# Kernel optimization log

Measured on AMD Instinct MI355X. Metric: run time of the kernel, lower is better.

The kernel has to match this reference:

```python
import jax, jax.numpy as jnp
import numpy as np


def _cos_map(N):
    # DCT-II basis: weight[n, x] = cos(n*(x+0.5)/N*pi)*sqrt(2/N), row 0 scaled by 1/sqrt(2)
    pos = (jnp.arange(N, dtype=jnp.float32) + 0.5) / N
    n = jnp.arange(N, dtype=jnp.float32)[:, None]
    w = jnp.cos(n * pos[None, :] * jnp.pi) * np.sqrt(2.0 / N)
    return w.at[0].multiply(1.0 / np.sqrt(2.0))


def _dct3(x, cT, cH, cW):
    # x: [B,C,T,H,W]; matmul(x, cos.T) along each axis
    x = jnp.einsum('bcthw,Ww->bcthW', x, cW)
    x = jnp.einsum('bcthw,Hh->bctHw', x, cH)
    x = jnp.einsum('bcthw,Tt->bcThw', x, cT)
    return x


def _idct3(x, cT, cH, cW):
    # matmul(x, cos) along each axis
    x = jnp.einsum('bcthw,wW->bcthW', x, cW)
    x = jnp.einsum('bcthw,hH->bctHw', x, cH)
    x = jnp.einsum('bcthw,tT->bcThw', x, cT)
    return x


def setup_inputs() -> dict:
    key = jax.random.key(0)
    ks = jax.random.split(key, 12)
    B, C, T, H, W = 2, 96, 16, 64, 64
    hd = 96
    s = 0.02
    return {
        'x': jax.random.normal(ks[0], (B, C, T, H, W), jnp.float32),
        'freq_embed': jax.random.normal(ks[1], (T, H, W, hd), jnp.float32),
        'dwconv_w': jax.random.normal(ks[2], (hd, 1, 3, 3, 3), jnp.float32) * s,
        'dwconv_b': jnp.zeros((hd,), jnp.float32),
        'linear_w': jax.random.normal(ks[3], (2 * hd, hd), jnp.float32) * s,
        'linear_b': jnp.zeros((2 * hd,), jnp.float32),
        'v0_w': jax.random.normal(ks[4], (hd, hd), jnp.float32) * s,
        'v0_b': jnp.zeros((hd,), jnp.float32),
        'tok_w': jax.random.normal(ks[5], (hd, hd), jnp.float32) * s,
        'tok_b': jnp.zeros((hd,), jnp.float32),
        'c': jnp.ones((1,), jnp.float32),
        'alpha': jnp.full((1,), 0.1, jnp.float32),
        'ln_g': jnp.ones((hd,), jnp.float32),
        'ln_b': jnp.zeros((hd,), jnp.float32),
        'out_w': jax.random.normal(ks[6], (hd, hd), jnp.float32) * s,
        'out_b': jnp.zeros((hd,), jnp.float32),
    }


def reference(x, freq_embed, dwconv_w, dwconv_b, linear_w, linear_b, v0_w, v0_b,
              tok_w, tok_b, c, alpha, ln_g, ln_b, out_w, out_b):
    B, C, T, H, W = x.shape
    hd = C
    # depthwise 3x3x3 conv
    y = jax.lax.conv_general_dilated(
        x, dwconv_w, (1, 1, 1), [(1, 1)] * 3,
        dimension_numbers=('NCDHW', 'OIDHW', 'NCDHW'), feature_group_count=hd)
    y = y + dwconv_b[None, :, None, None, None]
    yl = jnp.moveaxis(y, 1, -1)                     # [B,T,H,W,C]
    lin = yl @ linear_w.T + linear_b                # [B,T,H,W,2C]
    xg, z = jnp.split(lin, 2, axis=-1)
    v0 = xg @ v0_w.T + v0_b
    xc = jnp.moveaxis(xg, -1, 1)                    # [B,C,T,H,W]
    v0c = jnp.moveaxis(v0, -1, 1)
    cT, cH, cW = _cos_map(T), _cos_map(H), _cos_map(W)
    x_u0 = _dct3(xc, cT, cH, cW)
    x_v0 = _dct3(v0c, cT, cH, cW)
    # tau from freq_embed (exact GELU, as torch default)
    tau = jax.nn.gelu(freq_embed @ tok_w.T + tok_b, approximate=False)  # [T,H,W,C]
    tau = jnp.moveaxis(tau, -1, 0)[None]            # [1,C,T,H,W] broadcasts over B
    c_tau = c[0] * tau
    damping = jnp.exp(-alpha[0] / 2 * tau)
    spec = damping * (jnp.cos(c_tau) * x_u0 +
                      jnp.sin(c_tau) / (c[0] + 1e-8) * (x_v0 + alpha[0] / 2 * x_u0))
    xf = _idct3(spec, cT, cH, cW)
    xf = jnp.moveaxis(xf, 1, -1)                    # [B,T,H,W,C]
    mu = xf.mean(-1, keepdims=True)
    var = ((xf - mu) ** 2).mean(-1, keepdims=True)
    xf = (xf - mu) / jnp.sqrt(var + 1e-5) * ln_g + ln_b
    xf = xf * jax.nn.silu(z)                        # elementwise gate
    out = xf @ out_w.T + out_b
    return jnp.moveaxis(out, -1, 1)                 # [B,C,T,H,W]
```

## Files before the change

kernel.cpp:

```cpp
#include <hip/hip_runtime.h>
#include <math.h>

#define THW 65536
#define HW  4096
#define C96 96
#ifndef M_PI
#define M_PI 3.14159265358979323846
#endif

__global__ __launch_bounds__(256) void init_basis_k(float* __restrict__ b64,
                                                    float* __restrict__ b64T,
                                                    float* __restrict__ b16) {
  int tid = threadIdx.x;
  for (int i = tid; i < 4096; i += 256) {
    int n = i >> 6, x = i & 63;
    double s = sqrt(2.0 / 64.0) * (n == 0 ? sqrt(0.5) : 1.0);
    float v = (float)(cos((double)n * ((double)x + 0.5) * M_PI / 64.0) * s);
    b64[i] = v;
    b64T[x * 64 + n] = v;
  }
  {
    int n = tid >> 4, x = tid & 15;
    double s = sqrt(2.0 / 16.0) * (n == 0 ? sqrt(0.5) : 1.0);
    b16[tid & 255] = (float)(cos((double)n * ((double)x + 0.5) * M_PI / 16.0) * s);
  }
}

struct R3 { float a, b, c; };

#define LOADR(dst, row) { int rr_ = (row); int o_ = rr_ * 64 + lane; \
    dst.a = pmv[o_]; dst.b = pcv[o_]; dst.c = ppv[o_]; }

#define OUTROW(A, B, Cc, row) { \
    float P0, P1, P2; \
    P0 = w27[0]  * A.a;          P1 = w27[1]  * A.a;          P2 = w27[2]  * A.a; \
    P0 = fmaf(w27[3],  B.a, P0); P1 = fmaf(w27[4],  B.a, P1); P2 = fmaf(w27[5],  B.a, P2); \
    P0 = fmaf(w27[6],  Cc.a, P0); P1 = fmaf(w27[7],  Cc.a, P1); P2 = fmaf(w27[8],  Cc.a, P2); \
    P0 = fmaf(w27[9],  A.b, P0); P1 = fmaf(w27[10], A.b, P1); P2 = fmaf(w27[11], A.b, P2); \
    P0 = fmaf(w27[12], B.b, P0); P1 = fmaf(w27[13], B.b, P1); P2 = fmaf(w27[14], B.b, P2); \
    P0 = fmaf(w27[15], Cc.b, P0); P1 = fmaf(w27[16], Cc.b, P1); P2 = fmaf(w27[17], Cc.b, P2); \
    P0 = fmaf(w27[18], A.c, P0); P1 = fmaf(w27[19], A.c, P1); P2 = fmaf(w27[20], A.c, P2); \
    P0 = fmaf(w27[21], B.c, P0); P1 = fmaf(w27[22], B.c, P1); P2 = fmaf(w27[23], B.c, P2); \
    P0 = fmaf(w27[24], Cc.c, P0); P1 = fmaf(w27[25], Cc.c, P1); P2 = fmaf(w27[26], Cc.c, P2); \
    float lft = __shfl_up(P0, 1);  if (lane == 0)  lft = 0.f; \
    float rgt = __shfl_down(P2, 1); if (lane == 63) rgt = 0.f; \
    yp[(row) * 64] = bv + lft + P1 + rgt; }

__global__ __launch_bounds__(256) void dwconv_k(const float* __restrict__ x,
    const float* __restrict__ wv, const float* __restrict__ bias,
    float* __restrict__ y) {
  int lane = threadIdx.x & 63;
  int wvi  = threadIdx.x >> 6;
  int bc   = blockIdx.x;
  int t    = blockIdx.y * 4 + wvi;
  int h0   = blockIdx.z * 32;
  int c    = bc % C96;

  const float* pcv = x + (size_t)bc * THW + (size_t)t * HW;
  const float* pmv = (t > 0)  ? pcv - HW : pcv;
  const float* ppv = (t < 15) ? pcv + HW : pcv;

  float w27[27];
#pragma unroll
  for (int i = 0; i < 27; ++i) w27[i] = wv[c * 27 + i];
  if (t == 0) {
#pragma unroll
    for (int i = 0; i < 9; ++i) w27[i] = 0.f;
  }
  if (t == 15) {
#pragma unroll
    for (int i = 0; i < 9; ++i) w27[18 + i] = 0.f;
  }
  float bv = bias[c];
  float* yp = y + (size_t)bc * THW + (size_t)t * HW + lane;

  R3 s0, s1, s2, s3, n0, n1;
  if (h0 > 0) { LOADR(s0, h0 - 1) } else { s0.a = s0.b = s0.c = 0.f; }
  LOADR(s1, h0)
  LOADR(s2, h0 + 1)
  LOADR(s3, h0 + 2)
#pragma unroll
  for (int p = 0; p < 14; ++p) {
    int h = h0 + 2 * p;
    LOADR(n0, h + 3)
    LOADR(n1, h + 4)
    OUTROW(s0, s1, s2, h)
    OUTROW(s1, s2, s3, h + 1)
    s0 = s2; s1 = s3; s2 = n0; s3 = n1;
  }
  {
    int h = h0 + 28;
    LOADR(n0, h + 3)
    if (h0 == 0) { LOADR(n1, h + 4) }
    else { n1.a = n1.b = n1.c = 0.f; }
    OUTROW(s0, s1, s2, h)
    OUTROW(s1, s2, s3, h + 1)
    s0 = s2; s1 = s3; s2 = n0; s3 = n1;
  }
  {
    int h = h0 + 30;
    OUTROW(s0, s1, s2, h)
    OUTROW(s1, s2, s3, h + 1)
  }
}
#undef LOADR
#undef OUTROW

__global__ __launch_bounds__(256) void feT_k(const float* __restrict__ fe,
                                             float* __restrict__ feT) {
  __shared__ float t[96 * 65];
  int tid = threadIdx.x;
  int tok0 = blockIdx.x * 64;
  const float* p = fe + (size_t)tok0 * 96;
  for (int i = tid; i < 6144; i += 256) {
    int tok = i / 96;
    int ch = i - tok * 96;
    t[ch * 65 + tok] = p[i];
  }
  __syncthreads();
  for (int i = tid; i < 6144; i += 256) {
    int ch = i >> 6, tok = i & 63;
    feT[(size_t)ch * THW + tok0 + tok] = t[ch * 65 + tok];
  }
}

#define FMA4(A, WV) \
  A.x = fmaf(WV, v.x, A.x); A.y = fmaf(WV, v.y, A.y); \
  A.z = fmaf(WV, v.z, A.z); A.w = fmaf(WV, v.w, A.w);

#define WPAD 104
#define BK32 32

template <int EPI>
__global__ __launch_bounds__(512) void gemm96_k(
    const float* __restrict__ In, const float* __restrict__ W,
    const float* __restrict__ bias, float* __restrict__ Out,
    float* __restrict__ Out2, const float* __restrict__ zg,
    const float* __restrict__ lnG, const float* __restrict__ lnB,
    const float* __restrict__ scal_c, const float* __restrict__ scal_a,
    int N, size_t inStride, size_t outStride) {
  __shared__ float Wt[96 * WPAD];
  __shared__ float buf[BK32 * 256];
  int tid = threadIdx.x;
  int wvi = tid >> 6, ln = tid & 63;
  for (int i = tid; i < 2304; i += 512) {
    int k4 = i / 96, co = i - k4 * 96;
    float4 w4 = *(const float4*)(W + co * 96 + k4 * 4);
    int k = k4 * 4;
    Wt[(k + 0) * WPAD + co] = w4.x;
    Wt[(k + 1) * WPAD + co] = w4.y;
    Wt[(k + 2) * WPAD + co] = w4.z;
    Wt[(k + 3) * WPAD + co] = w4.w;
  }
  int n0 = blockIdx.x * 256 + ln * 4;
  int co0 = wvi * 12;
  const float* ipb = In + blockIdx.y * inStride + blockIdx.x * 256 + ln * 4;
  const float* zpb = (EPI == 2) ? (zg + blockIdx.y * inStride + blockIdx.x * 256 + ln * 4)
                                : nullptr;

  float4 mu4, rs4;
  if (EPI == 2) {
    float4 sum = make_float4(0.f, 0.f, 0.f, 0.f);
    float4 sq  = make_float4(0.f, 0.f, 0.f, 0.f);
#pragma unroll 8
    for (int ci = 0; ci < 96; ++ci) {
      float4 t = *(const float4*)(ipb + (size_t)ci * N);
      sum.x += t.x; sum.y += t.y; sum.z += t.z; sum.w += t.w;
      sq.x = fmaf(t.x, t.x, sq.x); sq.y = fmaf(t.y, t.y, sq.y);
      sq.z = fmaf(t.z, t.z, sq.z); sq.w = fmaf(t.w, t.w, sq.w);
    }
    const float r96 = 1.0f / 96.0f;
    mu4.x = sum.x * r96; mu4.y = sum.y * r96; mu4.z = sum.z * r96; mu4.w = sum.w * r96;
    rs4.x = rsqrtf(fmaxf(sq.x * r96 - mu4.x * mu4.x, 0.f) + 1e-5f);
    rs4.y = rsqrtf(fmaxf(sq.y * r96 - mu4.y * mu4.y, 0.f) + 1e-5f);
    rs4.z = rsqrtf(fmaxf(sq.z * r96 - mu4.z * mu4.z, 0.f) + 1e-5f);
    rs4.w = rsqrtf(fmaxf(sq.w * r96 - mu4.w * mu4.w, 0.f) + 1e-5f);
  }

  float4 acc[12];
#pragma unroll
  for (int j = 0; j < 12; ++j) {
    float bj = bias[co0 + j];
    acc[j] = make_float4(bj, bj, bj, bj);
  }

#pragma unroll 1
  for (int kb = 0; kb < 3; ++kb) {
#pragma unroll
    for (int i = 0; i < 4; ++i) {
      int r = i * 8 + wvi;
      int k = kb * BK32 + r;
      float4 v4 = *(const float4*)(ipb + (size_t)k * N);
      if (EPI == 2) {
        float4 zz = *(const float4*)(zpb + (size_t)k * N);
        float lgk = lnG[k], lbk = lnB[k];
        float gx = zz.x * __builtin_amdgcn_rcpf(1.0f + __expf(-zz.x));
        float gy = zz.y * __builtin_amdgcn_rcpf(1.0f + __expf(-zz.y));
        float gz = zz.z * __builtin_amdgcn_rcpf(1.0f + __expf(-zz.z));
        float gw = zz.w * __builtin_amdgcn_rcpf(1.0f + __expf(-zz.w));
        v4.x = fmaf((v4.x - mu4.x) * rs4.x, lgk, lbk) * gx;
        v4.y = fmaf((v4.y - mu4.y) * rs4.y, lgk, lbk) * gy;
        v4.z = fmaf((v4.z - mu4.z) * rs4.z, lgk, lbk) * gz;
        v4.w = fmaf((v4.w - mu4.w) * rs4.w, lgk, lbk) * gw;
      }
      *(float4*)&buf[r * 256 + ln * 4] = v4;
    }
    __syncthreads();
#pragma unroll 8
    for (int kk = 0; kk < BK32; ++kk) {
      int k = kb * BK32 + kk;
      float4 v = *(const float4*)&buf[kk * 256 + ln * 4];
      const float4* wr = (const float4*)&Wt[k * WPAD + co0];
#pragma unroll
      for (int j = 0; j < 3; ++j) {
        float4 wvv = wr[j];
        FMA4(acc[4 * j + 0], wvv.x);
        FMA4(acc[4 * j + 1], wvv.y);
        FMA4(acc[4 * j + 2], wvv.z);
        FMA4(acc[4 * j + 3], wvv.w);
      }
    }
    __syncthreads();
  }

  if (EPI == 1) {
    float cv = scal_c[0], al = scal_a[0];
    float rc = 1.0f / (cv + 1e-8f);
#define TAUMAP(T, AA, BB) { \
    float tau = 0.5f * (T) * (1.0f + erff((T) * 0.70710678118654752f)); \
    float ct = cv * tau; \
    float damp = __expf(-0.5f * al * tau); \
    float sc = __sinf(ct), cc = __cosf(ct); \
    AA = damp * (cc + sc * al * 0.5f * rc); BB = damp * sc * rc; }
#pragma unroll 2
    for (int j = 0; j < 12; ++j) {
      float4 a4, b4;
      TAUMAP(acc[j].x, a4.x, b4.x);
      TAUMAP(acc[j].y, a4.y, b4.y);
      TAUMAP(acc[j].z, a4.z, b4.z);
      TAUMAP(acc[j].w, a4.w, b4.w);
      *(float4*)(Out  + (size_t)(co0 + j) * N + n0) = a4;
      *(float4*)(Out2 + (size_t)(co0 + j) * N + n0) = b4;
    }
#undef TAUMAP
  } else {
    float* op = Out + blockIdx.y * outStride + n0;
#pragma unroll
    for (int j = 0; j < 12; ++j)
      *(float4*)(op + (size_t)(co0 + j) * N) = acc[j];
  }
}

#define INIT1B(p, j, bp) float4 p##j; { float bj_ = bp[co0 + j]; \
    p##j = make_float4(bj_, bj_, bj_, bj_); }
#define INIT12B(p, bp) INIT1B(p,0,bp) INIT1B(p,1,bp) INIT1B(p,2,bp) \
    INIT1B(p,3,bp) INIT1B(p,4,bp) INIT1B(p,5,bp) INIT1B(p,6,bp) \
    INIT1B(p,7,bp) INIT1B(p,8,bp) INIT1B(p,9,bp) INIT1B(p,10,bp) INIT1B(p,11,bp)
#define FMAS12(p) \
  FMA4(p##0, w0.x); FMA4(p##1, w0.y); FMA4(p##2,  w0.z); FMA4(p##3,  w0.w); \
  FMA4(p##4, w1.x); FMA4(p##5, w1.y); FMA4(p##6,  w1.z); FMA4(p##7,  w1.w); \
  FMA4(p##8, w2.x); FMA4(p##9, w2.y); FMA4(p##10, w2.z); FMA4(p##11, w2.w);
#define ST1P(p, j, op) *(float4*)((op) + (size_t)(co0 + j) * N + n0) = p##j;
#define ST12P(p, op) ST1P(p,0,op) ST1P(p,1,op) ST1P(p,2,op) ST1P(p,3,op) \
    ST1P(p,4,op) ST1P(p,5,op) ST1P(p,6,op) ST1P(p,7,op) ST1P(p,8,op) \
    ST1P(p,9,op) ST1P(p,10,op) ST1P(p,11,op)

__global__ __launch_bounds__(512) void dual_lin_k(
    const float* __restrict__ In, const float* __restrict__ WA,
    const float* __restrict__ WB, const float* __restrict__ biasA,
    const float* __restrict__ biasB, float* __restrict__ OutA,
    float* __restrict__ OutB, int N, size_t inStride, size_t outStride) {
  __shared__ float WtA[96 * 96];
  __shared__ float WtB[96 * 96];
  __shared__ float buf[BK32 * 256];
  int tid = threadIdx.x;
  int wvi = tid >> 6, ln = tid & 63;
  for (int i = tid; i < 2304; i += 512) {
    int k4 = i / 96, co = i - k4 * 96;
    int k = k4 * 4;
    float4 a4 = *(const float4*)(WA + co * 96 + k4 * 4);
    WtA[(k + 0) * 96 + co] = a4.x;
    WtA[(k + 1) * 96 + co] = a4.y;
    WtA[(k + 2) * 96 + co] = a4.z;
    WtA[(k + 3) * 96 + co] = a4.w;
    float4 b4 = *(const float4*)(WB + co * 96 + k4 * 4);
    WtB[(k + 0) * 96 + co] = b4.x;
    WtB[(k + 1) * 96 + co] = b4.y;
    WtB[(k + 2) * 96 + co] = b4.z;
    WtB[(k + 3) * 96 + co] = b4.w;
  }
  int n0 = blockIdx.x * 256 + ln * 4;
  int co0 = wvi * 12;
  const float* ipb = In + blockIdx.y * inStride + n0;

  INIT12B(A, biasA) INIT12B(B, biasB)

#pragma unroll 1
  for (int kb = 0; kb < 3; ++kb) {
#pragma unroll
    for (int i = 0; i < 4; ++i) {
      int r = i * 8 + wvi;
      int k = kb * BK32 + r;
      *(float4*)&buf[r * 256 + ln * 4] = *(const float4*)(ipb + (size_t)k * N);
    }
    __syncthreads();
#pragma unroll 4
    for (int kk = 0; kk < BK32; ++kk) {
      int k = kb * BK32 + kk;
      float4 v = *(const float4*)&buf[kk * 256 + ln * 4];
      {
        const float4* wr = (const float4*)&WtA[k * 96 + co0];
        float4 w0 = wr[0], w1 = wr[1], w2 = wr[2];
        FMAS12(A)
      }
      {
        const float4* wr = (const float4*)&WtB[k * 96 + co0];
        float4 w0 = wr[0], w1 = wr[1], w2 = wr[2];
        FMAS12(B)
      }
    }
    __syncthreads();
  }

  float* opA = OutA + blockIdx.y * outStride;
  float* opB = OutB + blockIdx.y * outStride;
  ST12P(A, opA) ST12P(B, opB)
}

__global__ __launch_bounds__(256) void wh_k(const float* __restrict__ in,
    float* __restrict__ out, const float* __restrict__ basis) {
  __shared__ float Xs[64 * 65];
  int tid = threadIdx.x;
  int lane = tid & 63;
  int g0 = __builtin_amdgcn_readfirstlane((tid >> 6) * 16);
  const float* ip = in + (size_t)blockIdx.x * HW;
  float* op = out + (size_t)blockIdx.x * HW;

  for (int i = tid; i < 1024; i += 256) {
    int h = i >> 4, w0x = (i & 15) * 4;
    float4 v = *(const float4*)(ip + h * 64 + w0x);
    float* d = &Xs[h * 65 + w0x];
    d[0] = v.x; d[1] = v.y; d[2] = v.z; d[3] = v.w;
  }
  __syncthreads();

  float accp[16];
#pragma unroll
  for (int j = 0; j < 16; ++j) accp[j] = 0.f;
  {
    const float* xrow = &Xs[lane * 65];
#pragma unroll 4
    for (int w = 0; w < 64; ++w) {
      float xv = xrow[w];
      const float* bw = basis + w * 64 + g0;
      float4 b0 = *(const float4*)(bw);
      float4 b1 = *(const float4*)(bw + 4);
      float4 b2 = *(const float4*)(bw + 8);
      float4 b3 = *(const float4*)(bw + 12);
      accp[0]  = fmaf(xv, b0.x, accp[0]);  accp[1]  = fmaf(xv, b0.y, accp[1]);
      accp[2]  = fmaf(xv, b0.z, accp[2]);  accp[3]  = fmaf(xv, b0.w, accp[3]);
      accp[4]  = fmaf(xv, b1.x, accp[4]);  accp[5]  = fmaf(xv, b1.y, accp[5]);
      accp[6]  = fmaf(xv, b1.z, accp[6]);  accp[7]  = fmaf(xv, b1.w, accp[7]);
      accp[8]  = fmaf(xv, b2.x, accp[8]);  accp[9]  = fmaf(xv, b2.y, accp[9]);
      accp[10] = fmaf(xv, b2.z, accp[10]); accp[11] = fmaf(xv, b2.w, accp[11]);
      accp[12] = fmaf(xv, b3.x, accp[12]); accp[13] = fmaf(xv, b3.y, accp[13]);
      accp[14] = fmaf(xv, b3.z, accp[14]); accp[15] = fmaf(xv, b3.w, accp[15]);
    }
  }
  __syncthreads();
  {
    float* trow = &Xs[lane * 65 + g0];
#pragma unroll
    for (int j = 0; j < 16; ++j) trow[j] = accp[j];
  }
  __syncthreads();

  float acc2[16];
#pragma unroll
  for (int j = 0; j < 16; ++j) acc2[j] = 0.f;
#pragma unroll 4
  for (int h = 0; h < 64; ++h) {
    float tv = Xs[h * 65 + lane];
    const float* bw = basis + h * 64 + g0;
    float4 b0 = *(const float4*)(bw);
    float4 b1 = *(const float4*)(bw + 4);
    float4 b2 = *(const float4*)(bw + 8);
    float4 b3 = *(const float4*)(bw + 12);
    acc2[0]  = fmaf(tv, b0.x, acc2[0]);  acc2[1]  = fmaf(tv, b0.y, acc2[1]);
    acc2[2]  = fmaf(tv, b0.z, acc2[2]);  acc2[3]  = fmaf(tv, b0.w, acc2[3]);
    acc2[4]  = fmaf(tv, b1.x, acc2[4]);  acc2[5]  = fmaf(tv, b1.y, acc2[5]);
    acc2[6]  = fmaf(tv, b1.z, acc2[6]);  acc2[7]  = fmaf(tv, b1.w, acc2[7]);
    acc2[8]  = fmaf(tv, b2.x, acc2[8]);  acc2[9]  = fmaf(tv, b2.y, acc2[9]);
    acc2[10] = fmaf(tv, b2.z, acc2[10]); acc2[11] = fmaf(tv, b2.w, acc2[11]);
    acc2[12] = fmaf(tv, b3.x, acc2[12]); acc2[13] = fmaf(tv, b3.y, acc2[13]);
    acc2[14] = fmaf(tv, b3.z, acc2[14]); acc2[15] = fmaf(tv, b3.w, acc2[15]);
  }
#pragma unroll
  for (int j = 0; j < 16; ++j)
    op[(g0 + j) * 64 + lane] = acc2[j];
}

__global__ __launch_bounds__(256) void tspec_k(const float* __restrict__ U0,
    const float* __restrict__ V0, const float* __restrict__ A,
    const float* __restrict__ Bc, const float* __restrict__ b16,
    float* __restrict__ out) {
  __shared__ float bs[256];
  int tid = threadIdx.x;
  bs[tid] = b16[tid];
  __syncthreads();
  int hw = blockIdx.x * 256 + tid;
  int c = blockIdx.y, b = blockIdx.z;
  size_t base = ((size_t)(b * C96 + c) * 16) * HW + hw;
  int cbase = c * THW + hw;
  float ua[16], va[16];
  {
    float u[16];
#pragma unroll
    for (int t = 0; t < 16; ++t) u[t] = U0[base + t * HW];
#pragma unroll
    for (int n = 0; n < 16; ++n) {
      float s = 0.0f;
#pragma unroll
      for (int t = 0; t < 16; ++t) s = fmaf(bs[n * 16 + t], u[t], s);
      ua[n] = s;
    }
  }
  {
    float v[16];
#pragma unroll
    for (int t = 0; t < 16; ++t) v[t] = V0[base + t * HW];
#pragma unroll
    for (int n = 0; n < 16; ++n) {
      float s = 0.0f;
#pragma unroll
      for (int t = 0; t < 16; ++t) s = fmaf(bs[n * 16 + t], v[t], s);
      va[n] = s;
    }
  }
  float so[16];
#pragma unroll 4
  for (int n = 0; n < 16; ++n)
    so[n] = A[cbase + n * HW] * ua[n] + Bc[cbase + n * HW] * va[n];
#pragma unroll
  for (int t = 0; t < 16; ++t) {
    float s = 0.0f;
#pragma unroll
    for (int n = 0; n < 16; ++n) s = fmaf(so[n], bs[n * 16 + t], s);
    out[base + t * HW] = s;
  }
}

extern "C" void kernel_launch(void* const* d_in, const int* in_sizes, int n_in,
                              void* d_out, int out_size, void* d_ws, size_t ws_size,
                              hipStream_t stream) {
  const float* x    = (const float*)d_in[0];
  const float* fe   = (const float*)d_in[1];
  const float* dww  = (const float*)d_in[2];
  const float* dwb  = (const float*)d_in[3];
  const float* linW = (const float*)d_in[4];
  const float* linB = (const float*)d_in[5];
  const float* v0W  = (const float*)d_in[6];
  const float* v0B  = (const float*)d_in[7];
  const float* tokW = (const float*)d_in[8];
  const float* tokB = (const float*)d_in[9];
  const float* cS   = (const float*)d_in[10];
  const float* aS   = (const float*)d_in[11];
  const float* lnG  = (const float*)d_in[12];
  const float* lnBp = (const float*)d_in[13];
  const float* outW = (const float*)d_in[14];
  const float* outB = (const float*)d_in[15];
  float* out = (float*)d_out;

  float* w = (float*)d_ws;
  const size_t TEN = (size_t)2 * C96 * THW;
  const size_t BST = (size_t)C96 * THW;
  float* b64    = w;
  float* b64T   = w + 4096;
  float* b16    = w + 8192;
  float* buf_y  = w + 16384;
  float* buf_xg = buf_y + TEN;
  float* buf_z  = buf_xg + TEN;
  float* buf_v0 = buf_z + TEN;
  float* bufA   = buf_v0 + TEN;
  float* bufB   = bufA + BST;
  size_t need = (size_t)(16384 + 4 * TEN + 2 * BST) * sizeof(float);
  if (ws_size < need) return;

  hipLaunchKernelGGL(init_basis_k, dim3(1), dim3(256), 0, stream, b64, b64T, b16);
  hipLaunchKernelGGL(dwconv_k, dim3(192, 4, 2), dim3(256), 0, stream, x, dww, dwb, buf_y);
  hipLaunchKernelGGL(dual_lin_k, dim3(256, 2), dim3(512), 0, stream,
                     buf_y, linW, linW + 9216, linB, linB + 96,
                     buf_xg, buf_z, THW, BST, BST);
  hipLaunchKernelGGL(feT_k, dim3(1024), dim3(256), 0, stream, fe, buf_v0);
  hipLaunchKernelGGL((gemm96_k<1>), dim3(256, 1), dim3(512), 0, stream,
                     buf_v0, tokW, tokB, bufA, bufB, (const float*)nullptr,
                     (const float*)nullptr, (const float*)nullptr,
                     cS, aS, THW, (size_t)0, (size_t)0);
  hipLaunchKernelGGL((gemm96_k<0>), dim3(256, 2), dim3(512), 0, stream,
                     buf_xg, v0W, v0B, buf_v0, (float*)nullptr, (const float*)nullptr,
                     (const float*)nullptr, (const float*)nullptr,
                     (const float*)nullptr, (const float*)nullptr, THW, BST, BST);
  hipLaunchKernelGGL(wh_k, dim3(3072), dim3(256), 0, stream, buf_xg, buf_y, b64T);
  hipLaunchKernelGGL(wh_k, dim3(3072), dim3(256), 0, stream, buf_v0, buf_xg, b64T);
  hipLaunchKernelGGL(tspec_k, dim3(16, 96, 2), dim3(256), 0, stream, buf_y, buf_xg, bufA, bufB, b16, buf_v0);
  hipLaunchKernelGGL(wh_k, dim3(3072), dim3(256), 0, stream, buf_v0, buf_y, b64);
  hipLaunchKernelGGL((gemm96_k<2>), dim3(256, 2), dim3(512), 0, stream,
                     buf_y, outW, outB, out, (float*)nullptr, buf_z,
                     lnG, lnBp, (const float*)nullptr, (const float*)nullptr, THW, BST, BST);
}
```

Before: 531.2 us.

## Fuse v0 projection into the dual linear kernel as a chained GEMM

The separate v0 GEMM launch, which re-read xg from global memory, is folded into the linear kernel. Each block keeps its xg accumulators in registers, stages them through shared memory in 32-channel chunks, reloads the shared weight tile with v0_w, and computes v0 directly. This removes one full read of the xg tensor and one launch, at the cost of extra syncs and a longer-running kernel with higher register pressure. The launch order is also moved so the freq_embed/tau kernels run before dwconv.

```diff
diff --git a/kernel.cpp b/kernel.cpp
--- a/kernel.cpp
+++ b/kernel.cpp
@@ -256,20 +256,27 @@
 #define INIT12B(p, bp) INIT1B(p,0,bp) INIT1B(p,1,bp) INIT1B(p,2,bp) \
     INIT1B(p,3,bp) INIT1B(p,4,bp) INIT1B(p,5,bp) INIT1B(p,6,bp) \
     INIT1B(p,7,bp) INIT1B(p,8,bp) INIT1B(p,9,bp) INIT1B(p,10,bp) INIT1B(p,11,bp)
-#define FMAS12(p) \
-  FMA4(p##0, w0.x); FMA4(p##1, w0.y); FMA4(p##2,  w0.z); FMA4(p##3,  w0.w); \
-  FMA4(p##4, w1.x); FMA4(p##5, w1.y); FMA4(p##6,  w1.z); FMA4(p##7,  w1.w); \
-  FMA4(p##8, w2.x); FMA4(p##9, w2.y); FMA4(p##10, w2.z); FMA4(p##11, w2.w);
-#define ST1P(p, j, op) *(float4*)((op) + (size_t)(co0 + j) * N + n0) = p##j;
-#define ST12P(p, op) ST1P(p,0,op) ST1P(p,1,op) ST1P(p,2,op) ST1P(p,3,op) \
-    ST1P(p,4,op) ST1P(p,5,op) ST1P(p,6,op) ST1P(p,7,op) ST1P(p,8,op) \
-    ST1P(p,9,op) ST1P(p,10,op) ST1P(p,11,op)
-
-__global__ __launch_bounds__(512) void dual_lin_k(
+#define FMAS12W(p, W0, W1, W2) \
+  FMA4(p##0, W0.x); FMA4(p##1, W0.y); FMA4(p##2,  W0.z); FMA4(p##3,  W0.w); \
+  FMA4(p##4, W1.x); FMA4(p##5, W1.y); FMA4(p##6,  W1.z); FMA4(p##7,  W1.w); \
+  FMA4(p##8, W2.x); FMA4(p##9, W2.y); FMA4(p##10, W2.z); FMA4(p##11, W2.w);
+#define ST1P(p, j, op, off) \
+    *(float4*)((op) + (size_t)(co0 + j) * N + (off)) = p##j;
+#define ST12P(p, op, off) ST1P(p,0,op,off) ST1P(p,1,op,off) ST1P(p,2,op,off) \
+    ST1P(p,3,op,off) ST1P(p,4,op,off) ST1P(p,5,op,off) ST1P(p,6,op,off) \
+    ST1P(p,7,op,off) ST1P(p,8,op,off) ST1P(p,9,op,off) ST1P(p,10,op,off) \
+    ST1P(p,11,op,off)
+
+#define STAGEA(j) { int r_ = co0 + j; if ((r_ >> 5) == q) \
+    *(float4*)&buf[(r_ & 31) * 256 + ln * 4] = A##j; }
+
+__global__ __launch_bounds__(512) void trip_lin_k(
     const float* __restrict__ In, const float* __restrict__ WA,
-    const float* __restrict__ WB, const float* __restrict__ biasA,
-    const float* __restrict__ biasB, float* __restrict__ OutA,
-    float* __restrict__ OutB, int N, size_t inStride, size_t outStride) {
+    const float* __restrict__ WB, const float* __restrict__ WV,
+    const float* __restrict__ biasA, const float* __restrict__ biasB,
+    const float* __restrict__ biasV, float* __restrict__ OutA,
+    float* __restrict__ OutB, float* __restrict__ OutV,
+    int N, size_t inStride, size_t outStride) {
   __shared__ float WtA[96 * 96];
   __shared__ float WtB[96 * 96];
   __shared__ float buf[BK32 * 256];
@@ -311,12 +318,12 @@
       {
         const float4* wr = (const float4*)&WtA[k * 96 + co0];
         float4 w0 = wr[0], w1 = wr[1], w2 = wr[2];
-        FMAS12(A)
+        FMAS12W(A, w0, w1, w2)
       }
       {
         const float4* wr = (const float4*)&WtB[k * 96 + co0];
         float4 w0 = wr[0], w1 = wr[1], w2 = wr[2];
-        FMAS12(B)
+        FMAS12W(B, w0, w1, w2)
       }
     }
     __syncthreads();
@@ -324,7 +331,39 @@
 
   float* opA = OutA + blockIdx.y * outStride;
   float* opB = OutB + blockIdx.y * outStride;
-  ST12P(A, opA) ST12P(B, opB)
+  ST12P(B, opB, n0)
+  ST12P(A, opA, n0)
+
+  for (int i = tid; i < 2304; i += 512) {
+    int k4 = i / 96, co = i - k4 * 96;
+    int k = k4 * 4;
+    float4 v4 = *(const float4*)(WV + co * 96 + k4 * 4);
+    WtA[(k + 0) * 96 + co] = v4.x;
+    WtA[(k + 1) * 96 + co] = v4.y;
+    WtA[(k + 2) * 96 + co] = v4.z;
+    WtA[(k + 3) * 96 + co] = v4.w;
+  }
+  INIT12B(V, biasV)
+  __syncthreads();
+
+#pragma unroll 1
+  for (int q = 0; q < 3; ++q) {
+    STAGEA(0) STAGEA(1) STAGEA(2) STAGEA(3) STAGEA(4)  STAGEA(5)
+    STAGEA(6) STAGEA(7) STAGEA(8) STAGEA(9) STAGEA(10) STAGEA(11)
+    __syncthreads();
+#pragma unroll 4
+    for (int kk = 0; kk < BK32; ++kk) {
+      int k = q * BK32 + kk;
+      float4 v = *(const float4*)&buf[kk * 256 + ln * 4];
+      const float4* wr = (const float4*)&WtA[k * 96 + co0];
+      float4 w0 = wr[0], w1 = wr[1], w2 = wr[2];
+      FMAS12W(V, w0, w1, w2)
+    }
+    __syncthreads();
+  }
+
+  float* opV = OutV + blockIdx.y * outStride;
+  ST12P(V, opV, n0)
 }
 
 __global__ __launch_bounds__(256) void wh_k(const float* __restrict__ in,
@@ -487,19 +526,15 @@
   if (ws_size < need) return;
 
   hipLaunchKernelGGL(init_basis_k, dim3(1), dim3(256), 0, stream, b64, b64T, b16);
-  hipLaunchKernelGGL(dwconv_k, dim3(192, 4, 2), dim3(256), 0, stream, x, dww, dwb, buf_y);
-  hipLaunchKernelGGL(dual_lin_k, dim3(256, 2), dim3(512), 0, stream,
-                     buf_y, linW, linW + 9216, linB, linB + 96,
-                     buf_xg, buf_z, THW, BST, BST);
   hipLaunchKernelGGL(feT_k, dim3(1024), dim3(256), 0, stream, fe, buf_v0);
   hipLaunchKernelGGL((gemm96_k<1>), dim3(256, 1), dim3(512), 0, stream,
                      buf_v0, tokW, tokB, bufA, bufB, (const float*)nullptr,
                      (const float*)nullptr, (const float*)nullptr,
                      cS, aS, THW, (size_t)0, (size_t)0);
-  hipLaunchKernelGGL((gemm96_k<0>), dim3(256, 2), dim3(512), 0, stream,
-                     buf_xg, v0W, v0B, buf_v0, (float*)nullptr, (const float*)nullptr,
-                     (const float*)nullptr, (const float*)nullptr,
-                     (const float*)nullptr, (const float*)nullptr, THW, BST, BST);
+  hipLaunchKernelGGL(dwconv_k, dim3(192, 4, 2), dim3(256), 0, stream, x, dww, dwb, buf_y);
+  hipLaunchKernelGGL(trip_lin_k, dim3(256, 2), dim3(512), 0, stream,
+                     buf_y, linW, linW + 9216, v0W, linB, linB + 96, v0B,
+                     buf_xg, buf_z, buf_v0, THW, BST, BST);
   hipLaunchKernelGGL(wh_k, dim3(3072), dim3(256), 0, stream, buf_xg, buf_y, b64T);
   hipLaunchKernelGGL(wh_k, dim3(3072), dim3(256), 0, stream, buf_v0, buf_xg, b64T);
   hipLaunchKernelGGL(tspec_k, dim3(16, 96, 2), dim3(256), 0, stream, buf_y, buf_xg, bufA, bufB, b16, buf_v0);
```

After: 544.7 us. +2.5%, slower.
